# Kernel optimization log

Measured on AMD Instinct MI355X. Metric: run time of the kernel, lower is better.

The kernel has to match this reference:

```python
import jax, jax.numpy as jnp
import numpy as np

# FlowNetC correlation config (matches init_kwargs)
PAD = 20           # pad_size
MAX_DISP = 20      # max_displacement
STRIDE2 = 2        # displacement stride
K = 1              # kernel_size (1x1 patch)
# stride1 = 1, corr_multiply = 1 (multiply mode)

GRID_RAD = MAX_DISP // STRIDE2           # 10
N_DISP = (2 * GRID_RAD + 1) ** 2         # 441 output channels


def _disp_offsets():
    # slice start offsets into the padded input2 for each displacement
    # (dy, dx) in {-GRID_RAD..GRID_RAD} * STRIDE2; start = PAD + d (pad == max_disp)
    d = np.arange(-GRID_RAD, GRID_RAD + 1) * STRIDE2
    dy, dx = np.meshgrid(d, d, indexing='ij')  # row-major: dy outer, dx inner
    return np.stack([PAD + dy.ravel(), PAD + dx.ravel()], axis=1).astype(np.int32)  # [441,2]


def setup_inputs() -> dict:
    key = jax.random.key(0)
    k1, k2 = jax.random.split(key)
    B, C, H, W = 8, 256, 64, 64
    input1 = jax.random.normal(k1, (B, C, H, W), dtype=jnp.float32)
    input2 = jax.random.normal(k2, (B, C, H, W), dtype=jnp.float32)
    return {"input1": input1, "input2": input2}


def reference(input1, input2):
    B, C, H, W = input1.shape
    sumelems = float(K * K * C)  # normalization used by the CUDA kernel
    # zero-pad input2 spatially by PAD (pad_size == max_displacement)
    x2p = jnp.pad(input2, ((0, 0), (0, 0), (PAD, PAD), (PAD, PAD)))
    offs = jnp.asarray(_disp_offsets())  # [441, 2] int32

    def step(carry, off):
        # window of input2 displaced by (dy, dx) relative to input1
        sl = jax.lax.dynamic_slice(x2p, (0, 0, off[0], off[1]), (B, C, H, W))
        corr = jnp.sum(input1 * sl, axis=1) / sumelems  # [B, H, W]
        return carry, corr

    _, out = jax.lax.scan(step, None, offs)       # [441, B, H, W]
    return jnp.transpose(out, (1, 0, 2, 3))       # [B, 441, H, W]
```

## Files before the change

kernel.cpp:

```cpp
#include <hip/hip_runtime.h>
#include <hip/hip_bf16.h>


typedef short    bf16x8 __attribute__((ext_vector_type(8)));
typedef float    f32x4  __attribute__((ext_vector_type(4)));

constexpr int CSTRIDE = 64 * 64;
constexpr int BSTRIDE = 256 * CSTRIDE;

union BF2 { __hip_bfloat162 h; unsigned u; };
union BF1 { __hip_bfloat16 h; unsigned short u; };

__device__ inline unsigned pack_bf2(float lo, float hi) {
    BF2 cv;
    cv.h = __float22bfloat162_rn(make_float2(lo, hi));
    return cv.u;
}

__device__ __align__(16) const uint4 ZERO16 = {0u, 0u, 0u, 0u};

__global__ __launch_bounds__(256)
void conv_in2(const float* __restrict__ in2, unsigned* __restrict__ out_dw)
{
    __shared__ unsigned short lt[64 * 66];
    const int tid = threadIdx.x;
    const int b = blockIdx.x & 7;
    const int y = blockIdx.x >> 3;
    const float* src = in2 + b * BSTRIDE + y * 64;
    unsigned* odw = out_dw + (b * 64 + y) * 8192;

    for (int c0 = 0; c0 < 256; c0 += 64) {
        __syncthreads();
#pragma unroll
        for (int it = 0; it < 16; ++it) {
            const int c = it * 4 + (tid >> 6);
            const int x = tid & 63;
            BF1 cv; cv.h = __float2bfloat16(src[(c0 + c) * CSTRIDE + x]);
            lt[x * 66 + c] = cv.u;
        }
        __syncthreads();
        const unsigned* ldw = reinterpret_cast<const unsigned*>(lt);
#pragma unroll
        for (int it = 0; it < 8; ++it) {
            const int d   = tid + 256 * it;
            const int c8g = d >> 8;
            const int x   = (d >> 2) & 63;
            const int cd2 = d & 3;
            odw[((c0 >> 3) + c8g) * 256 + x * 4 + cd2] = ldw[x * 33 + c8g * 4 + cd2];
        }
    }
}

__global__ __launch_bounds__(1024, 4)
void corr_mfma(const float* __restrict__ in1,
               const uint4* __restrict__ in2t,
               float* __restrict__ out)
{
    __shared__ float slds[2][21 * 65];

    const int tid  = threadIdx.x;
    const int lane = tid & 63;
    const int w    = tid >> 6;
    const int cl   = lane & 15;
    const int q    = lane >> 4;
    const int m    = w & 3;
    const int n    = m + (w >> 2);
    const int b    = blockIdx.x & 7;
    const int p    = blockIdx.x >> 3;
    const int y0   = 4 * (p >> 1) + (p & 1);

    bf16x8 af[2][8];
#pragma unroll
    for (int h = 0; h < 2; ++h) {
        const float* pb = in1 + b * BSTRIDE + (y0 + 2 * h) * 64 + 16 * m + cl
                        + 8 * q * CSTRIDE;
#pragma unroll
        for (int k = 0; k < 8; ++k) {
            const float* pp = pb + 32 * k * CSTRIDE;
            float v[8];
#pragma unroll
            for (int j = 0; j < 8; ++j) v[j] = pp[j * CSTRIDE];
#pragma unroll
            for (int j = 0; j < 4; ++j)
                ((unsigned*)&af[h][k])[j] = pack_bf2(v[2 * j], v[2 * j + 1]);
        }
    }

    const int  x    = 16 * n + cl - 20;
    const bool xok  = (x >= 0) && (x < 64);
    const int  gcol = 16 * n + cl;

    for (int i = 0; i < 22; ++i) {
        const int  yy      = y0 - 20 + 2 * i;
        const bool compute = (yy >= 0) && (yy < 64);

        if (compute) {
            const uint4* src = in2t + (b * 64 + yy) * 2048 + x;
            f32x4 acc0 = {0.f, 0.f, 0.f, 0.f};
            f32x4 acc1 = {0.f, 0.f, 0.f, 0.f};
#pragma unroll
            for (int k = 0; k < 8; ++k) {
                const uint4* pk = xok ? (src + (4 * k + q) * 64) : &ZERO16;
                const uint4  wv = *pk;
                const bf16x8 bf = __builtin_bit_cast(bf16x8, wv);
                acc0 = __builtin_amdgcn_mfma_f32_16x16x32_bf16(af[0][k], bf, acc0, 0, 0, 0);
                acc1 = __builtin_amdgcn_mfma_f32_16x16x32_bf16(af[1][k], bf, acc1, 0, 0, 0);
            }
#pragma unroll
            for (int i4 = 0; i4 < 4; ++i4) {
                const int gx = 16 * m + 4 * q + i4;
                const int d2 = gcol - gx;
                if (d2 >= 0 && d2 <= 40 && !(d2 & 1)) {
                    slds[0][(d2 >> 1) * 65 + gx] = acc0[i4];
                    slds[1][(d2 >> 1) * 65 + gx] = acc1[i4];
                }
            }
        }
        __syncthreads();

        const int r0 = i, r1 = i - 1;
#pragma unroll
        for (int t3 = 0; t3 < 3; ++t3) {
            const int t = tid + 1024 * t3;
            if (t < 2 * 21 * 64) {
                const int h  = (t >= 1344) ? 1 : 0;
                const int u  = t - 1344 * h;
                const int dx = u >> 6, gx = u & 63;
                const int r  = h ? r1 : r0;
                if (r >= 0 && r <= 20) {
                    const float val = compute ? slds[h][dx * 65 + gx] * (1.f / 256.f)
                                              : 0.f;
                    out[((b * 441 + r * 21 + dx) * 64 + y0 + 2 * h) * 64 + gx] = val;
                }
            }
        }
        __syncthreads();
    }
}

extern "C" void kernel_launch(void* const* d_in, const int* in_sizes, int n_in,
                              void* d_out, int out_size, void* d_ws, size_t ws_size,
                              hipStream_t stream) {
    const float* in1 = (const float*)d_in[0];
    const float* in2 = (const float*)d_in[1];
    float* out = (float*)d_out;

    conv_in2<<<dim3(512), dim3(256), 0, stream>>>(in2, (unsigned*)d_ws);
    corr_mfma<<<dim3(256), dim3(1024), 0, stream>>>(in1, (const uint4*)d_ws, out);
}
```

Baseline: 151.1 us.

## Prefetch in2 rows into LDS with async double buffering

Each converted in2 row is staged into a zero-padded LDS row buffer using global_load_lds, issuing the next row's load while the current row is used by the MFMA loop. This removes redundant per-wave global loads and out-of-range pointer selects, and hides load latency behind compute. The result scratch is also double-buffered, which lets one of the two barriers per iteration go. In exchange, LDS use rises to roughly 136KB per block, and correctness depends on the async LDS loads being waited on before the barrier.

```diff
diff --git a/kernel.cpp b/kernel.cpp
--- a/kernel.cpp
+++ b/kernel.cpp
@@ -7,6 +7,7 @@
 
 constexpr int CSTRIDE = 64 * 64;
 constexpr int BSTRIDE = 256 * CSTRIDE;
+constexpr int CW      = 112;
 
 union BF2 { __hip_bfloat162 h; unsigned u; };
 union BF1 { __hip_bfloat16 h; unsigned short u; };
@@ -16,8 +17,6 @@
     cv.h = __float22bfloat162_rn(make_float2(lo, hi));
     return cv.u;
 }
-
-__device__ __align__(16) const uint4 ZERO16 = {0u, 0u, 0u, 0u};
 
 __global__ __launch_bounds__(256)
 void conv_in2(const float* __restrict__ in2, unsigned* __restrict__ out_dw)
@@ -56,7 +55,8 @@
                const uint4* __restrict__ in2t,
                float* __restrict__ out)
 {
-    __shared__ float slds[2][21 * 65];
+    __shared__ uint4 rowbuf[2][32 * CW];
+    __shared__ float slds[2][2][21 * 65];
 
     const int tid  = threadIdx.x;
     const int lane = tid & 63;
@@ -66,8 +66,8 @@
     const int m    = w & 3;
     const int n    = m + (w >> 2);
     const int b    = blockIdx.x & 7;
-    const int p    = blockIdx.x >> 3;
-    const int y0   = 4 * (p >> 1) + (p & 1);
+    const int pp   = blockIdx.x >> 3;
+    const int y0   = 4 * (pp >> 1) + (pp & 1);
 
     bf16x8 af[2][8];
 #pragma unroll
@@ -76,32 +76,67 @@
                         + 8 * q * CSTRIDE;
 #pragma unroll
         for (int k = 0; k < 8; ++k) {
-            const float* pp = pb + 32 * k * CSTRIDE;
+            const float* ppk = pb + 32 * k * CSTRIDE;
             float v[8];
 #pragma unroll
-            for (int j = 0; j < 8; ++j) v[j] = pp[j * CSTRIDE];
+            for (int j = 0; j < 8; ++j) v[j] = ppk[j * CSTRIDE];
 #pragma unroll
             for (int j = 0; j < 4; ++j)
                 ((unsigned*)&af[h][k])[j] = pack_bf2(v[2 * j], v[2 * j + 1]);
         }
     }
 
-    const int  x    = 16 * n + cl - 20;
-    const bool xok  = (x >= 0) && (x < 64);
-    const int  gcol = 16 * n + cl;
+    for (int t = tid; t < 2 * 32 * 48; t += 1024) {
+        const int bi = t / 1536;
+        const int u  = t - bi * 1536;
+        const int c8 = u / 48;
+        const int j  = u - c8 * 48;
+        const int xp = (j < 20) ? j : (j + 64);
+        rowbuf[bi][c8 * CW + xp] = make_uint4(0u, 0u, 0u, 0u);
+    }
+
+    {
+        const int yy = y0 - 20;
+        if (yy >= 0 && yy < 64) {
+#pragma unroll
+            for (int j = 0; j < 2; ++j) {
+                const int c8 = 2 * w + j;
+                const unsigned* g = reinterpret_cast<const unsigned*>(
+                    in2t + (b * 64 + yy) * 2048 + c8 * 64 + lane);
+                uint4* l = &rowbuf[0][c8 * CW + 20 + lane];
+                __builtin_amdgcn_global_load_lds(
+                    (const __attribute__((address_space(1))) unsigned*)g,
+                    (__attribute__((address_space(3))) unsigned*)l, 16, 0, 0);
+            }
+        }
+    }
+    __syncthreads();
 
     for (int i = 0; i < 22; ++i) {
-        const int  yy      = y0 - 20 + 2 * i;
-        const bool compute = (yy >= 0) && (yy < 64);
+        const int  yy   = y0 - 20 + 2 * i;
+        const bool comp = (yy >= 0) && (yy < 64);
+        const int  pb   = i & 1;
 
-        if (compute) {
-            const uint4* src = in2t + (b * 64 + yy) * 2048 + x;
+        const int yn = yy + 2;
+        if (i + 1 < 22 && yn >= 0 && yn < 64) {
+#pragma unroll
+            for (int j = 0; j < 2; ++j) {
+                const int c8 = 2 * w + j;
+                const unsigned* g = reinterpret_cast<const unsigned*>(
+                    in2t + (b * 64 + yn) * 2048 + c8 * 64 + lane);
+                uint4* l = &rowbuf[1 - pb][c8 * CW + 20 + lane];
+                __builtin_amdgcn_global_load_lds(
+                    (const __attribute__((address_space(1))) unsigned*)g,
+                    (__attribute__((address_space(3))) unsigned*)l, 16, 0, 0);
+            }
+        }
+
+        if (comp) {
             f32x4 acc0 = {0.f, 0.f, 0.f, 0.f};
             f32x4 acc1 = {0.f, 0.f, 0.f, 0.f};
 #pragma unroll
             for (int k = 0; k < 8; ++k) {
-                const uint4* pk = xok ? (src + (4 * k + q) * 64) : &ZERO16;
-                const uint4  wv = *pk;
+                const uint4  wv = rowbuf[pb][(4 * k + q) * CW + 16 * n + cl];
                 const bf16x8 bf = __builtin_bit_cast(bf16x8, wv);
                 acc0 = __builtin_amdgcn_mfma_f32_16x16x32_bf16(af[0][k], bf, acc0, 0, 0, 0);
                 acc1 = __builtin_amdgcn_mfma_f32_16x16x32_bf16(af[1][k], bf, acc1, 0, 0, 0);
@@ -109,10 +144,10 @@
 #pragma unroll
             for (int i4 = 0; i4 < 4; ++i4) {
                 const int gx = 16 * m + 4 * q + i4;
-                const int d2 = gcol - gx;
+                const int d2 = (16 * n + cl) - gx;
                 if (d2 >= 0 && d2 <= 40 && !(d2 & 1)) {
-                    slds[0][(d2 >> 1) * 65 + gx] = acc0[i4];
-                    slds[1][(d2 >> 1) * 65 + gx] = acc1[i4];
+                    slds[pb][0][(d2 >> 1) * 65 + gx] = acc0[i4];
+                    slds[pb][1][(d2 >> 1) * 65 + gx] = acc1[i4];
                 }
             }
         }
@@ -128,13 +163,12 @@
                 const int dx = u >> 6, gx = u & 63;
                 const int r  = h ? r1 : r0;
                 if (r >= 0 && r <= 20) {
-                    const float val = compute ? slds[h][dx * 65 + gx] * (1.f / 256.f)
-                                              : 0.f;
+                    const float val = comp ? slds[pb][h][dx * 65 + gx] * (1.f / 256.f)
+                                           : 0.f;
                     out[((b * 441 + r * 21 + dx) * 64 + y0 + 2 * h) * 64 + gx] = val;
                 }
             }
         }
-        __syncthreads();
     }
 }
 
```

After: 165.1 us. 1.09x slower.
